# Optimization experiments

Hardware: AMD Instinct MI355X
Metric: run time of the kernel (lower is better)

## Reference

```python
import jax, jax.numpy as jnp
import numpy as np

N = 200000      # total nodes
B = 1024        # graphs
D = 256         # node_dim
OUT = 256       # out_dim


def setup_inputs() -> dict:
    key = jax.random.key(0)
    ks = jax.random.split(key, 16)
    x = jax.random.normal(ks[0], (N, D), dtype=jnp.float32)
    # sorted segment ids covering all B graphs (no empty segments)
    extra = jax.random.randint(ks[1], (N - B,), 0, B)
    batch = jnp.sort(jnp.concatenate([jnp.arange(B, dtype=jnp.int32), extra.astype(jnp.int32)]))
    # one-hot node type mask [N, 3]
    types = jax.random.randint(ks[2], (N,), 0, 3)
    node_type_mask = jax.nn.one_hot(types, 3, dtype=jnp.int32)
    s = 1.0 / np.sqrt(D)
    # attn_weight: Linear(D, D//2) -> Tanh -> Linear(D//2, 1)
    aw1 = jax.random.uniform(ks[3], (D, D // 2), jnp.float32, -s, s)
    ab1 = jnp.zeros((D // 2,), jnp.float32)
    aw2 = jax.random.uniform(ks[4], (D // 2, 1), jnp.float32, -s, s)
    ab2 = jnp.zeros((1,), jnp.float32)
    # three typed transforms Linear(D, D)
    we = jax.random.uniform(ks[5], (D, D), jnp.float32, -s, s)
    be = jnp.zeros((D,), jnp.float32)
    wv = jax.random.uniform(ks[6], (D, D), jnp.float32, -s, s)
    bv = jnp.zeros((D,), jnp.float32)
    wp = jax.random.uniform(ks[7], (D, D), jnp.float32, -s, s)
    bp = jnp.zeros((D,), jnp.float32)
    # readout MLP: Linear(3D, 2*OUT) -> SiLU -> (Dropout eval) -> Linear(2*OUT, OUT)
    w1 = jax.random.uniform(ks[8], (3 * D, 2 * OUT), jnp.float32, -1.0 / np.sqrt(3 * D), 1.0 / np.sqrt(3 * D))
    b1 = jnp.zeros((2 * OUT,), jnp.float32)
    w2 = jax.random.uniform(ks[9], (2 * OUT, OUT), jnp.float32, -1.0 / np.sqrt(2 * OUT), 1.0 / np.sqrt(2 * OUT))
    b2 = jnp.zeros((OUT,), jnp.float32)
    return dict(x=x, batch=batch, node_type_mask=node_type_mask, num_segments=B,
                aw1=aw1, ab1=ab1, aw2=aw2, ab2=ab2, we=we, be=be, wv=wv, bv=bv,
                wp=wp, bp=bp, w1=w1, b1=b1, w2=w2, b2=b2)


def reference(x, batch, node_type_mask, num_segments,
              aw1, ab1, aw2, ab2, we, be, wv, bv, wp, bp, w1, b1, w2, b2):
    nseg = int(num_segments)
    # global_mean_pool
    counts = jax.ops.segment_sum(jnp.ones((x.shape[0],), x.dtype), batch, num_segments=nseg)
    mean_pool = jax.ops.segment_sum(x, batch, num_segments=nseg) / counts[:, None]
    # attention scores + segment softmax
    scores = jnp.tanh(x @ aw1 + ab1) @ aw2 + ab2            # [N, 1]
    s = scores[:, 0]
    m = jax.ops.segment_max(s, batch, num_segments=nseg)    # [B]
    e = jnp.exp(s - m[batch])
    z = jax.ops.segment_sum(e, batch, num_segments=nseg)
    attn = e / z[batch]                                     # [N]
    attn_pool = jax.ops.segment_sum(x * attn[:, None], batch, num_segments=nseg)
    # typed physical pooling (node_type_mask path)
    mask = node_type_mask.astype(x.dtype)
    typed_x = (mask[:, 0:1] * (x @ we + be)
               + mask[:, 1:2] * (x @ wv + bv)
               + mask[:, 2:3] * (x @ wp + bp))
    phys_pool = jax.ops.segment_sum(typed_x, batch, num_segments=nseg)
    combined = jnp.concatenate([mean_pool, attn_pool, phys_pool], axis=-1)  # [B, 3D]
    h = jax.nn.silu(combined @ w1 + b1)                     # dropout = identity (eval)
    return h @ w2 + b2                                      # [B, OUT]
```

## Files before the change

### kernel.cpp

```cpp
#include <hip/hip_runtime.h>

typedef float  f32x4  __attribute__((ext_vector_type(4)));
typedef short  s16x8  __attribute__((ext_vector_type(8)));
typedef short  s16x4  __attribute__((ext_vector_type(4)));

__device__ __forceinline__ short f2bf(float f) {
  unsigned u = __float_as_uint(f);
  u += 0x7fffu + ((u >> 16) & 1u);
  return (short)(u >> 16);
}
__device__ __forceinline__ float bf2f(unsigned short us) {
  return __uint_as_float(((unsigned)us) << 16);
}
__device__ __forceinline__ float tanh_fast(float x) {
  const float e = __expf(2.0f * x);
  return 1.0f - 2.0f / (e + 1.0f);
}

__global__ __launch_bounds__(256) void k_cvtw(
    const float* __restrict__ aw1, const float* __restrict__ we, const float* __restrict__ wv,
    const float* __restrict__ wp, const float* __restrict__ w1, const float* __restrict__ w2,
    unsigned short* __restrict__ Awt, unsigned short* __restrict__ Wpt,
    unsigned short* __restrict__ W1t, unsigned short* __restrict__ W2t) {
  const int b = blockIdx.x, tid = threadIdx.x;
  if (b < 128) {
    const int e = b * 256 + tid, n = e >> 8, k = e & 255;
    Awt[e] = (unsigned short)f2bf(aw1[k * 128 + n]);
  } else if (b < 896) {
    const int e = (b - 128) * 256 + tid, n = e / 768, k = e % 768;
    const int part = k >> 8, kk = k & 255;
    const float* W = (part == 0) ? we : ((part == 1) ? wv : wp);
    Wpt[e] = (unsigned short)f2bf(W[kk * 256 + n]);
  } else if (b < 2432) {
    const int e = (b - 896) * 256 + tid, n = e / 768, k = e % 768;
    W1t[e] = (unsigned short)f2bf(w1[k * 512 + n]);
  } else {
    const int e = (b - 2432) * 256 + tid, n = e >> 9, k = e & 511;
    W2t[e] = (unsigned short)f2bf(w2[k * 256 + n]);
  }
}

__global__ __launch_bounds__(256) void k_score_pool(
    const float* __restrict__ x, const int* __restrict__ batch, const int* __restrict__ mask,
    const unsigned short* __restrict__ Awt, const float* __restrict__ ab1,
    const float* __restrict__ aw2, const float* __restrict__ ab2,
    float* __restrict__ P, float* __restrict__ EX, float* __restrict__ ZC,
    int nnodes) {
  __shared__ __align__(16) short xs[2][32][264];
  __shared__ __align__(16) float sred[4][32];
  __shared__ __align__(16) float e_sh[4][32];
  __shared__ int st_all[320];

  const int tid  = threadIdx.x;
  const int lane = tid & 63;
  const int w    = tid >> 6;
  const int quad = lane >> 4;
  const int l15  = lane & 15;

  s16x8 bfrag[8][2];
  float ab1v[2], aw2v[2];
#pragma unroll
  for (int ct = 0; ct < 2; ++ct) {
    const int col = w * 32 + ct * 16 + l15;
    ab1v[ct] = ab1[col];
    aw2v[ct] = aw2[col];
    const s16x8* bp = reinterpret_cast<const s16x8*>(Awt + (size_t)col * 256);
#pragma unroll
    for (int kt = 0; kt < 8; ++kt) bfrag[kt][ct] = bp[kt * 4 + quad];
  }
  const float ab2v = ab2[0];

  const int tiles = nnodes >> 5;
  const int tpb   = (tiles + (int)gridDim.x - 1) / (int)gridDim.x;
  const int t_beg = blockIdx.x * tpb;
  const int t_end = min(t_beg + tpb, tiles);
  if (t_beg >= t_end) return;

  {
    const int nodes0 = t_beg * 32, nblk = (t_end - t_beg) * 32;
    for (int i = tid; i < nblk; i += 256) {
      const int g = nodes0 + i;
      st_all[i] = batch[g] * 4 + mask[g * 3 + 1] + 2 * mask[g * 3 + 2];
    }
  }

  f32x4 stg[8];
  auto load_regs = [&](int tile) {
    const f32x4* xp = reinterpret_cast<const f32x4*>(x + (size_t)tile * 8192);
#pragma unroll
    for (int i = 0; i < 8; ++i) stg[i] = xp[tid + 256 * i];
  };
  const int col4 = (tid & 63) * 4;
  auto cvt_write = [&](int b) {
#pragma unroll
    for (int i = 0; i < 8; ++i) {
      const int row = (tid >> 6) + 4 * i;
      s16x4 v; v[0] = f2bf(stg[i][0]); v[1] = f2bf(stg[i][1]);
      v[2] = f2bf(stg[i][2]); v[3] = f2bf(stg[i][3]);
      *reinterpret_cast<s16x4*>(&xs[b][row][col4]) = v;
    }
  };

  load_regs(t_beg);
  cvt_write(0);
  __syncthreads();

  float a0 = 0.f, a1 = 0.f, a2 = 0.f, aex = 0.f, zc = 0.f;
  int cur = -1;

  auto flush = [&]() {
    atomicAdd(&P[cur * 768 + tid], a0);
    atomicAdd(&P[cur * 768 + 256 + tid], a1);
    atomicAdd(&P[cur * 768 + 512 + tid], a2);
    atomicAdd(&EX[cur * 256 + tid], aex);
    if (tid < 4) atomicAdd(&ZC[cur * 4 + tid], zc);
    a0 = a1 = a2 = aex = zc = 0.f;
  };

  for (int tile = t_beg; tile < t_end; ++tile) {
    const int buf = (tile - t_beg) & 1;
    const bool more = (tile + 1 < t_end);
    if (more) load_regs(tile + 1);

#pragma unroll
    for (int ng = 0; ng < 2; ++ng) {
      s16x8 af[8];
#pragma unroll
      for (int kt = 0; kt < 8; ++kt)
        af[kt] = *reinterpret_cast<const s16x8*>(&xs[buf][16 * ng + l15][kt * 32 + quad * 8]);
      float part[4] = {0.f, 0.f, 0.f, 0.f};
#pragma unroll
      for (int ct = 0; ct < 2; ++ct) {
        f32x4 acc = {0.f, 0.f, 0.f, 0.f};
#pragma unroll
        for (int kt = 0; kt < 8; ++kt)
          acc = __builtin_amdgcn_mfma_f32_16x16x32_bf16(af[kt], bfrag[kt][ct], acc, 0, 0, 0);
#pragma unroll
        for (int r = 0; r < 4; ++r)
          part[r] += tanh_fast(acc[r] + ab1v[ct]) * aw2v[ct];
      }
#pragma unroll
      for (int off = 1; off < 16; off <<= 1) {
#pragma unroll
        for (int r = 0; r < 4; ++r) part[r] += __shfl_xor(part[r], off);
      }
      if (l15 == 0) {
#pragma unroll
        for (int r = 0; r < 4; ++r) sred[w][16 * ng + quad * 4 + r] = part[r];
      }
    }
    __syncthreads();

    if (lane < 32) {
      const float s = ab2v + sred[0][lane] + sred[1][lane] + sred[2][lane] + sred[3][lane];
      e_sh[w][lane] = __expf(s);
    }

    const int base = (tile - t_beg) * 32;
#pragma unroll
    for (int n = 0; n < 32; ++n) {
      const int st  = st_all[base + n];
      const int seg = st >> 2, t = st & 3;
      if (seg != cur) { if (cur >= 0) flush(); cur = seg; }
      const float e  = e_sh[w][n];
      const float xv = bf2f((unsigned short)xs[buf][n][tid]);
      aex += e * xv;
      if (t == 0) a0 += xv; else if (t == 1) a1 += xv; else a2 += xv;
      if (tid < 4) zc += (tid == 0) ? e : ((t == tid - 1) ? 1.f : 0.f);
    }

    if (more) cvt_write(buf ^ 1);
    __syncthreads();
  }
  if (cur >= 0) flush();
}

__global__ __launch_bounds__(256) void k_finalize(
    const float* __restrict__ P, const float* __restrict__ EX,
    const float* __restrict__ ZC, float* __restrict__ comb) {
  const int b = blockIdx.x, d = threadIdx.x;
  const float p0 = P[b * 768 + d], p1 = P[b * 768 + 256 + d], p2 = P[b * 768 + 512 + d];
  const float cnt = ZC[b * 4 + 1] + ZC[b * 4 + 2] + ZC[b * 4 + 3];
  comb[(size_t)b * 768 + d]       = (p0 + p1 + p2) / cnt;
  comb[(size_t)b * 768 + 256 + d] = EX[b * 256 + d] / ZC[b * 4];
}

__global__ __launch_bounds__(256) void k_phys(
    const float* __restrict__ P, const unsigned short* __restrict__ Wpt,
    const float* __restrict__ be, const float* __restrict__ bv, const float* __restrict__ bp,
    const float* __restrict__ ZC, float* __restrict__ comb) {
  __shared__ __align__(16) short as16[16][776];
  const int tid = threadIdx.x, lane = tid & 63, w = tid >> 6;
  const int quad = lane >> 4, l15 = lane & 15;
  const int rowbase = blockIdx.x * 16;
  const int col = blockIdx.y * 64 + w * 16 + l15;

  s16x8 bfr[24];
  const s16x8* bpf = reinterpret_cast<const s16x8*>(Wpt + (size_t)col * 768);
#pragma unroll
  for (int kt = 0; kt < 24; ++kt) bfr[kt] = bpf[kt * 4 + quad];

  const f32x4* ap = reinterpret_cast<const f32x4*>(P + (size_t)rowbase * 768);
#pragma unroll
  for (int i = 0; i < 12; ++i) {
    const int ci = tid + 256 * i;
    f32x4 v = ap[ci];
    const int row = ci / 192, c4 = (ci % 192) * 4;
    s16x4 b; b[0] = f2bf(v[0]); b[1] = f2bf(v[1]); b[2] = f2bf(v[2]); b[3] = f2bf(v[3]);
    *reinterpret_cast<s16x4*>(&as16[row][c4]) = b;
  }
  __syncthreads();

  f32x4 acc = {0.f, 0.f, 0.f, 0.f};
#pragma unroll
  for (int kt = 0; kt < 24; ++kt) {
    s16x8 af = *reinterpret_cast<const s16x8*>(&as16[l15][kt * 32 + quad * 8]);
    acc = __builtin_amdgcn_mfma_f32_16x16x32_bf16(af, bfr[kt], acc, 0, 0, 0);
  }
  const float ben = be[col], bvn = bv[col], bpn = bp[col];
#pragma unroll
  for (int r = 0; r < 4; ++r) {
    const int row = rowbase + quad * 4 + r;
    const float v = acc[r] + ZC[row * 4 + 1] * ben + ZC[row * 4 + 2] * bvn + ZC[row * 4 + 3] * bpn;
    comb[(size_t)row * 768 + 512 + col] = v;
  }
}

__global__ __launch_bounds__(256) void k_mlp1(
    const float* __restrict__ A, const unsigned short* __restrict__ W1t,
    const float* __restrict__ b1, float* __restrict__ H) {
  __shared__ __align__(16) short as16[16][776];
  const int tid = threadIdx.x, lane = tid & 63, w = tid >> 6;
  const int quad = lane >> 4, l15 = lane & 15;
  const int rowbase = blockIdx.x * 16;
  const int col = blockIdx.y * 64 + w * 16 + l15;

  s16x8 bfr[24];
  const s16x8* bpf = reinterpret_cast<const s16x8*>(W1t + (size_t)col * 768);
#pragma unroll
  for (int kt = 0; kt < 24; ++kt) bfr[kt] = bpf[kt * 4 + quad];

  const f32x4* ap = reinterpret_cast<const f32x4*>(A + (size_t)rowbase * 768);
#pragma unroll
  for (int i = 0; i < 12; ++i) {
    const int ci = tid + 256 * i;
    f32x4 v = ap[ci];
    const int row = ci / 192, c4 = (ci % 192) * 4;
    s16x4 b; b[0] = f2bf(v[0]); b[1] = f2bf(v[1]); b[2] = f2bf(v[2]); b[3] = f2bf(v[3]);
    *reinterpret_cast<s16x4*>(&as16[row][c4]) = b;
  }
  __syncthreads();

  f32x4 acc = {0.f, 0.f, 0.f, 0.f};
#pragma unroll
  for (int kt = 0; kt < 24; ++kt) {
    s16x8 af = *reinterpret_cast<const s16x8*>(&as16[l15][kt * 32 + quad * 8]);
    acc = __builtin_amdgcn_mfma_f32_16x16x32_bf16(af, bfr[kt], acc, 0, 0, 0);
  }
  const float bn = b1[col];
#pragma unroll
  for (int r = 0; r < 4; ++r) {
    const int row = rowbase + quad * 4 + r;
    const float v = acc[r] + bn;
    H[(size_t)row * 512 + col] = v / (1.f + __expf(-v));
  }
}

__global__ __launch_bounds__(256) void k_mlp2(
    const float* __restrict__ A, const unsigned short* __restrict__ W2t,
    const float* __restrict__ b2, float* __restrict__ out) {
  __shared__ __align__(16) short as16[16][520];
  const int tid = threadIdx.x, lane = tid & 63, w = tid >> 6;
  const int quad = lane >> 4, l15 = lane & 15;
  const int rowbase = blockIdx.x * 16;
  const int col = blockIdx.y * 64 + w * 16 + l15;

  s16x8 bfr[16];
  const s16x8* bpf = reinterpret_cast<const s16x8*>(W2t + (size_t)col * 512);
#pragma unroll
  for (int kt = 0; kt < 16; ++kt) bfr[kt] = bpf[kt * 4 + quad];

  const f32x4* ap = reinterpret_cast<const f32x4*>(A + (size_t)rowbase * 512);
#pragma unroll
  for (int i = 0; i < 8; ++i) {
    const int ci = tid + 256 * i;
    f32x4 v = ap[ci];
    const int row = ci >> 7, c4 = (ci & 127) * 4;
    s16x4 b; b[0] = f2bf(v[0]); b[1] = f2bf(v[1]); b[2] = f2bf(v[2]); b[3] = f2bf(v[3]);
    *reinterpret_cast<s16x4*>(&as16[row][c4]) = b;
  }
  __syncthreads();

  f32x4 acc = {0.f, 0.f, 0.f, 0.f};
#pragma unroll
  for (int kt = 0; kt < 16; ++kt) {
    s16x8 af = *reinterpret_cast<const s16x8*>(&as16[l15][kt * 32 + quad * 8]);
    acc = __builtin_amdgcn_mfma_f32_16x16x32_bf16(af, bfr[kt], acc, 0, 0, 0);
  }
  const float bn = b2[col];
#pragma unroll
  for (int r = 0; r < 4; ++r) {
    const int row = rowbase + quad * 4 + r;
    out[(size_t)row * 256 + col] = acc[r] + bn;
  }
}

extern "C" void kernel_launch(void* const* d_in, const int* in_sizes, int n_in,
                              void* d_out, int out_size, void* d_ws, size_t ws_size,
                              hipStream_t stream) {
  const float* x    = (const float*)d_in[0];
  const int*   batch= (const int*)  d_in[1];
  const int*   mask = (const int*)  d_in[2];
  const float* aw1  = (const float*)d_in[4];
  const float* ab1  = (const float*)d_in[5];
  const float* aw2  = (const float*)d_in[6];
  const float* ab2  = (const float*)d_in[7];
  const float* we   = (const float*)d_in[8];
  const float* be   = (const float*)d_in[9];
  const float* wv   = (const float*)d_in[10];
  const float* bv   = (const float*)d_in[11];
  const float* wp   = (const float*)d_in[12];
  const float* bp   = (const float*)d_in[13];
  const float* w1   = (const float*)d_in[14];
  const float* b1   = (const float*)d_in[15];
  const float* w2   = (const float*)d_in[16];
  const float* b2   = (const float*)d_in[17];
  float* out = (float*)d_out;
  const int nn = in_sizes[1];

  float* ws = (float*)d_ws;
  float* P    = ws;
  float* EXs  = P    + 786432;
  float* ZCs  = EXs  + 262144;
  float* comb = ZCs  + 4096;
  float* hbuf = comb + 786432;
  unsigned short* Awt = (unsigned short*)(hbuf + 524288);
  unsigned short* Wpt = Awt + 32768;
  unsigned short* W1t = Wpt + 196608;
  unsigned short* W2t = W1t + 393216;

  hipMemsetAsync(P, 0, (size_t)(786432 + 262144 + 4096) * sizeof(float), stream);

  k_cvtw      <<<2944, 256, 0, stream>>>(aw1, we, wv, wp, w1, w2, Awt, Wpt, W1t, W2t);
  k_score_pool<<<1024, 256, 0, stream>>>(x, batch, mask, Awt, ab1, aw2, ab2, P, EXs, ZCs, nn);
  k_finalize  <<<1024, 256, 0, stream>>>(P, EXs, ZCs, comb);
  k_phys      <<<dim3(64, 4), 256, 0, stream>>>(P, Wpt, be, bv, bp, ZCs, comb);
  k_mlp1      <<<dim3(64, 8), 256, 0, stream>>>(comb, W1t, b1, hbuf);
  k_mlp2      <<<dim3(64, 4), 256, 0, stream>>>(hbuf, W2t, b2, out);
}
```

Before: 371.4 us.

## Fuse finalize, typed-phys GEMM and readout MLP into one tail kernel

Replaces the four post-pooling kernels (finalize, phys GEMM, MLP layer 1, MLP layer 2) with a single 512-thread kernel per 16-row tile. Intermediates (combined features and hidden activations) stay in LDS as bf16 instead of round-tripping through global memory. This removes three launches and the comb/hbuf traffic. In exchange, only 64 blocks run, each looping over all output columns, which lowers parallelism across the GPU.

```diff
diff --git a/kernel.cpp b/kernel.cpp
--- a/kernel.cpp
+++ b/kernel.cpp
@@ -175,133 +175,113 @@
   if (cur >= 0) flush();
 }
 
-__global__ __launch_bounds__(256) void k_finalize(
-    const float* __restrict__ P, const float* __restrict__ EX,
-    const float* __restrict__ ZC, float* __restrict__ comb) {
-  const int b = blockIdx.x, d = threadIdx.x;
-  const float p0 = P[b * 768 + d], p1 = P[b * 768 + 256 + d], p2 = P[b * 768 + 512 + d];
-  const float cnt = ZC[b * 4 + 1] + ZC[b * 4 + 2] + ZC[b * 4 + 3];
-  comb[(size_t)b * 768 + d]       = (p0 + p1 + p2) / cnt;
-  comb[(size_t)b * 768 + 256 + d] = EX[b * 256 + d] / ZC[b * 4];
-}
-
-__global__ __launch_bounds__(256) void k_phys(
-    const float* __restrict__ P, const unsigned short* __restrict__ Wpt,
+__global__ __launch_bounds__(512) void k_tail(
+    const float* __restrict__ P, const float* __restrict__ EX, const float* __restrict__ ZC,
+    const unsigned short* __restrict__ Wpt, const unsigned short* __restrict__ W1t,
+    const unsigned short* __restrict__ W2t,
     const float* __restrict__ be, const float* __restrict__ bv, const float* __restrict__ bp,
-    const float* __restrict__ ZC, float* __restrict__ comb) {
-  __shared__ __align__(16) short as16[16][776];
+    const float* __restrict__ b1, const float* __restrict__ b2,
+    float* __restrict__ out) {
+  __shared__ __align__(16) short asP[16][776];
+  __shared__ __align__(16) short asC[16][776];
+  __shared__ __align__(16) short ash[16][520];
+
   const int tid = threadIdx.x, lane = tid & 63, w = tid >> 6;
   const int quad = lane >> 4, l15 = lane & 15;
   const int rowbase = blockIdx.x * 16;
-  const int col = blockIdx.y * 64 + w * 16 + l15;
-
-  s16x8 bfr[24];
-  const s16x8* bpf = reinterpret_cast<const s16x8*>(Wpt + (size_t)col * 768);
-#pragma unroll
-  for (int kt = 0; kt < 24; ++kt) bfr[kt] = bpf[kt * 4 + quad];
 
   const f32x4* ap = reinterpret_cast<const f32x4*>(P + (size_t)rowbase * 768);
 #pragma unroll
-  for (int i = 0; i < 12; ++i) {
-    const int ci = tid + 256 * i;
+  for (int i = 0; i < 6; ++i) {
+    const int ci = tid + 512 * i;
     f32x4 v = ap[ci];
     const int row = ci / 192, c4 = (ci % 192) * 4;
     s16x4 b; b[0] = f2bf(v[0]); b[1] = f2bf(v[1]); b[2] = f2bf(v[2]); b[3] = f2bf(v[3]);
-    *reinterpret_cast<s16x4*>(&as16[row][c4]) = b;
+    *reinterpret_cast<s16x4*>(&asP[row][c4]) = b;
   }
   __syncthreads();
 
-  f32x4 acc = {0.f, 0.f, 0.f, 0.f};
-#pragma unroll
-  for (int kt = 0; kt < 24; ++kt) {
-    s16x8 af = *reinterpret_cast<const s16x8*>(&as16[l15][kt * 32 + quad * 8]);
-    acc = __builtin_amdgcn_mfma_f32_16x16x32_bf16(af, bfr[kt], acc, 0, 0, 0);
-  }
-  const float ben = be[col], bvn = bv[col], bpn = bp[col];
-#pragma unroll
-  for (int r = 0; r < 4; ++r) {
-    const int row = rowbase + quad * 4 + r;
-    const float v = acc[r] + ZC[row * 4 + 1] * ben + ZC[row * 4 + 2] * bvn + ZC[row * 4 + 3] * bpn;
-    comb[(size_t)row * 768 + 512 + col] = v;
-  }
-}
-
-__global__ __launch_bounds__(256) void k_mlp1(
-    const float* __restrict__ A, const unsigned short* __restrict__ W1t,
-    const float* __restrict__ b1, float* __restrict__ H) {
-  __shared__ __align__(16) short as16[16][776];
-  const int tid = threadIdx.x, lane = tid & 63, w = tid >> 6;
-  const int quad = lane >> 4, l15 = lane & 15;
-  const int rowbase = blockIdx.x * 16;
-  const int col = blockIdx.y * 64 + w * 16 + l15;
-
-  s16x8 bfr[24];
-  const s16x8* bpf = reinterpret_cast<const s16x8*>(W1t + (size_t)col * 768);
-#pragma unroll
-  for (int kt = 0; kt < 24; ++kt) bfr[kt] = bpf[kt * 4 + quad];
-
-  const f32x4* ap = reinterpret_cast<const f32x4*>(A + (size_t)rowbase * 768);
-#pragma unroll
-  for (int i = 0; i < 12; ++i) {
-    const int ci = tid + 256 * i;
-    f32x4 v = ap[ci];
-    const int row = ci / 192, c4 = (ci % 192) * 4;
-    s16x4 b; b[0] = f2bf(v[0]); b[1] = f2bf(v[1]); b[2] = f2bf(v[2]); b[3] = f2bf(v[3]);
-    *reinterpret_cast<s16x4*>(&as16[row][c4]) = b;
+  {
+    const int d  = tid & 255;
+    const int r0 = (tid >> 8) * 8;
+#pragma unroll
+    for (int rr = 0; rr < 8; ++rr) {
+      const int r = r0 + rr, row = rowbase + r;
+      const float z   = ZC[row * 4 + 0];
+      const float cnt = ZC[row * 4 + 1] + ZC[row * 4 + 2] + ZC[row * 4 + 3];
+      const float mp  = (P[(size_t)row * 768 + d] + P[(size_t)row * 768 + 256 + d] +
+                         P[(size_t)row * 768 + 512 + d]) / cnt;
+      const float at  = EX[(size_t)row * 256 + d] / z;
+      asC[r][d]       = f2bf(mp);
+      asC[r][256 + d] = f2bf(at);
+    }
+  }
+
+#pragma unroll 1
+  for (int cg = 0; cg < 2; ++cg) {
+    const int col = cg * 128 + w * 16 + l15;
+    s16x8 bfr[24];
+    const s16x8* bpf = reinterpret_cast<const s16x8*>(Wpt + (size_t)col * 768);
+#pragma unroll
+    for (int kt = 0; kt < 24; ++kt) bfr[kt] = bpf[kt * 4 + quad];
+    f32x4 acc = {0.f, 0.f, 0.f, 0.f};
+#pragma unroll
+    for (int kt = 0; kt < 24; ++kt) {
+      s16x8 af = *reinterpret_cast<const s16x8*>(&asP[l15][kt * 32 + quad * 8]);
+      acc = __builtin_amdgcn_mfma_f32_16x16x32_bf16(af, bfr[kt], acc, 0, 0, 0);
+    }
+    const float ben = be[col], bvn = bv[col], bpn = bp[col];
+#pragma unroll
+    for (int r = 0; r < 4; ++r) {
+      const int rl = quad * 4 + r, row = rowbase + rl;
+      const float v = acc[r] + ZC[row * 4 + 1] * ben + ZC[row * 4 + 2] * bvn + ZC[row * 4 + 3] * bpn;
+      asC[rl][512 + col] = f2bf(v);
+    }
   }
   __syncthreads();
 
-  f32x4 acc = {0.f, 0.f, 0.f, 0.f};
-#pragma unroll
-  for (int kt = 0; kt < 24; ++kt) {
-    s16x8 af = *reinterpret_cast<const s16x8*>(&as16[l15][kt * 32 + quad * 8]);
-    acc = __builtin_amdgcn_mfma_f32_16x16x32_bf16(af, bfr[kt], acc, 0, 0, 0);
-  }
-  const float bn = b1[col];
-#pragma unroll
-  for (int r = 0; r < 4; ++r) {
-    const int row = rowbase + quad * 4 + r;
-    const float v = acc[r] + bn;
-    H[(size_t)row * 512 + col] = v / (1.f + __expf(-v));
-  }
-}
-
-__global__ __launch_bounds__(256) void k_mlp2(
-    const float* __restrict__ A, const unsigned short* __restrict__ W2t,
-    const float* __restrict__ b2, float* __restrict__ out) {
-  __shared__ __align__(16) short as16[16][520];
-  const int tid = threadIdx.x, lane = tid & 63, w = tid >> 6;
-  const int quad = lane >> 4, l15 = lane & 15;
-  const int rowbase = blockIdx.x * 16;
-  const int col = blockIdx.y * 64 + w * 16 + l15;
-
-  s16x8 bfr[16];
-  const s16x8* bpf = reinterpret_cast<const s16x8*>(W2t + (size_t)col * 512);
-#pragma unroll
-  for (int kt = 0; kt < 16; ++kt) bfr[kt] = bpf[kt * 4 + quad];
-
-  const f32x4* ap = reinterpret_cast<const f32x4*>(A + (size_t)rowbase * 512);
-#pragma unroll
-  for (int i = 0; i < 8; ++i) {
-    const int ci = tid + 256 * i;
-    f32x4 v = ap[ci];
-    const int row = ci >> 7, c4 = (ci & 127) * 4;
-    s16x4 b; b[0] = f2bf(v[0]); b[1] = f2bf(v[1]); b[2] = f2bf(v[2]); b[3] = f2bf(v[3]);
-    *reinterpret_cast<s16x4*>(&as16[row][c4]) = b;
+#pragma unroll 1
+  for (int cg = 0; cg < 4; ++cg) {
+    const int col = cg * 128 + w * 16 + l15;
+    s16x8 bfr[24];
+    const s16x8* bpf = reinterpret_cast<const s16x8*>(W1t + (size_t)col * 768);
+#pragma unroll
+    for (int kt = 0; kt < 24; ++kt) bfr[kt] = bpf[kt * 4 + quad];
+    f32x4 acc = {0.f, 0.f, 0.f, 0.f};
+#pragma unroll
+    for (int kt = 0; kt < 24; ++kt) {
+      s16x8 af = *reinterpret_cast<const s16x8*>(&asC[l15][kt * 32 + quad * 8]);
+      acc = __builtin_amdgcn_mfma_f32_16x16x32_bf16(af, bfr[kt], acc, 0, 0, 0);
+    }
+    const float bn = b1[col];
+#pragma unroll
+    for (int r = 0; r < 4; ++r) {
+      const int rl = quad * 4 + r;
+      const float v = acc[r] + bn;
+      ash[rl][col] = f2bf(v / (1.f + __expf(-v)));
+    }
   }
   __syncthreads();
 
-  f32x4 acc = {0.f, 0.f, 0.f, 0.f};
-#pragma unroll
-  for (int kt = 0; kt < 16; ++kt) {
-    s16x8 af = *reinterpret_cast<const s16x8*>(&as16[l15][kt * 32 + quad * 8]);
-    acc = __builtin_amdgcn_mfma_f32_16x16x32_bf16(af, bfr[kt], acc, 0, 0, 0);
-  }
-  const float bn = b2[col];
-#pragma unroll
-  for (int r = 0; r < 4; ++r) {
-    const int row = rowbase + quad * 4 + r;
-    out[(size_t)row * 256 + col] = acc[r] + bn;
+#pragma unroll 1
+  for (int cg = 0; cg < 2; ++cg) {
+    const int col = cg * 128 + w * 16 + l15;
+    s16x8 bfr[16];
+    const s16x8* bpf = reinterpret_cast<const s16x8*>(W2t + (size_t)col * 512);
+#pragma unroll
+    for (int kt = 0; kt < 16; ++kt) bfr[kt] = bpf[kt * 4 + quad];
+    f32x4 acc = {0.f, 0.f, 0.f, 0.f};
+#pragma unroll
+    for (int kt = 0; kt < 16; ++kt) {
+      s16x8 af = *reinterpret_cast<const s16x8*>(&ash[l15][kt * 32 + quad * 8]);
+      acc = __builtin_amdgcn_mfma_f32_16x16x32_bf16(af, bfr[kt], acc, 0, 0, 0);
+    }
+    const float bn = b2[col];
+#pragma unroll
+    for (int r = 0; r < 4; ++r) {
+      const int rl = quad * 4 + r;
+      out[(size_t)(rowbase + rl) * 256 + col] = acc[r] + bn;
+    }
   }
 }
 
@@ -332,9 +312,7 @@
   float* P    = ws;
   float* EXs  = P    + 786432;
   float* ZCs  = EXs  + 262144;
-  float* comb = ZCs  + 4096;
-  float* hbuf = comb + 786432;
-  unsigned short* Awt = (unsigned short*)(hbuf + 524288);
+  unsigned short* Awt = (unsigned short*)(ZCs + 4096);
   unsigned short* Wpt = Awt + 32768;
   unsigned short* W1t = Wpt + 196608;
   unsigned short* W2t = W1t + 393216;
@@ -343,8 +321,5 @@
 
   k_cvtw      <<<2944, 256, 0, stream>>>(aw1, we, wv, wp, w1, w2, Awt, Wpt, W1t, W2t);
   k_score_pool<<<1024, 256, 0, stream>>>(x, batch, mask, Awt, ab1, aw2, ab2, P, EXs, ZCs, nn);
-  k_finalize  <<<1024, 256, 0, stream>>>(P, EXs, ZCs, comb);
-  k_phys      <<<dim3(64, 4), 256, 0, stream>>>(P, Wpt, be, bv, bp, ZCs, comb);
-  k_mlp1      <<<dim3(64, 8), 256, 0, stream>>>(comb, W1t, b1, hbuf);
-  k_mlp2      <<<dim3(64, 4), 256, 0, stream>>>(hbuf, W2t, b2, out);
-}
+  k_tail      <<<64, 512, 0, stream>>>(P, EXs, ZCs, Wpt, W1t, W2t, be, bv, bp, b1, b2, out);
+}
```

Result: slower. 395.6 us (+6.5%).

## Compute segment pooling sums with MFMA over one-hot and exp-weight matrices

Applied to the files above, without the earlier changes.

Replaces the scalar per-node accumulation loop in the score/pool kernel with bf16 MFMA. A small left matrix of exp weights (split hi/lo for precision) and one-hot type indicators multiplies a transposed bf16 copy of the x tile. Each run of nodes in the same segment is handled by masking the weight matrix with a ballot-derived range, and the z/count terms are reduced with shuffles and popcounts. It also single-buffers the MFMA A tile, adds a double-buffered transposed layout, balances the tile split across blocks, and sets launch bounds for two blocks per CU. The cost is extra LDS traffic for the transposed writes and bf16 rounding in the mean and typed sums.

```diff
diff --git a/kernel.cpp b/kernel.cpp
--- a/kernel.cpp
+++ b/kernel.cpp
@@ -40,15 +40,16 @@
   }
 }
 
-__global__ __launch_bounds__(256) void k_score_pool(
+__global__ __launch_bounds__(256, 2) void k_score_pool(
     const float* __restrict__ x, const int* __restrict__ batch, const int* __restrict__ mask,
     const unsigned short* __restrict__ Awt, const float* __restrict__ ab1,
     const float* __restrict__ aw2, const float* __restrict__ ab2,
     float* __restrict__ P, float* __restrict__ EX, float* __restrict__ ZC,
     int nnodes) {
-  __shared__ __align__(16) short xs[2][32][264];
+  __shared__ __align__(16) short xs[32][264];
+  __shared__ __align__(16) short xsB[2][8192];
   __shared__ __align__(16) float sred[4][32];
-  __shared__ __align__(16) float e_sh[4][32];
+  __shared__ __align__(16) short em[16][40];
   __shared__ int st_all[320];
 
   const int tid  = threadIdx.x;
@@ -71,9 +72,8 @@
   const float ab2v = ab2[0];
 
   const int tiles = nnodes >> 5;
-  const int tpb   = (tiles + (int)gridDim.x - 1) / (int)gridDim.x;
-  const int t_beg = blockIdx.x * tpb;
-  const int t_end = min(t_beg + tpb, tiles);
+  const int t_beg = (int)(((long long)blockIdx.x * tiles) / (long long)gridDim.x);
+  const int t_end = (int)(((long long)(blockIdx.x + 1) * tiles) / (long long)gridDim.x);
   if (t_beg >= t_end) return;
 
   {
@@ -82,22 +82,33 @@
       const int g = nodes0 + i;
       st_all[i] = batch[g] * 4 + mask[g * 3 + 1] + 2 * mask[g * 3 + 2];
     }
+    for (int i = tid; i < 640; i += 256) (&em[0][0])[i] = 0;
   }
 
   f32x4 stg[8];
   auto load_regs = [&](int tile) {
     const f32x4* xp = reinterpret_cast<const f32x4*>(x + (size_t)tile * 8192);
 #pragma unroll
-    for (int i = 0; i < 8; ++i) stg[i] = xp[tid + 256 * i];
+    for (int i = 0; i < 8; ++i) stg[i] = xp[(8 * w + i) * 64 + lane];
   };
-  const int col4 = (tid & 63) * 4;
-  auto cvt_write = [&](int b) {
+  auto cvt_write = [&](int bB) {
+    s16x4 xv[8];
 #pragma unroll
     for (int i = 0; i < 8; ++i) {
-      const int row = (tid >> 6) + 4 * i;
-      s16x4 v; v[0] = f2bf(stg[i][0]); v[1] = f2bf(stg[i][1]);
-      v[2] = f2bf(stg[i][2]); v[3] = f2bf(stg[i][3]);
-      *reinterpret_cast<s16x4*>(&xs[b][row][col4]) = v;
+      xv[i][0] = f2bf(stg[i][0]); xv[i][1] = f2bf(stg[i][1]);
+      xv[i][2] = f2bf(stg[i][2]); xv[i][3] = f2bf(stg[i][3]);
+    }
+#pragma unroll
+    for (int i = 0; i < 8; ++i)
+      *reinterpret_cast<s16x4*>(&xs[8 * w + i][lane * 4]) = xv[i];
+    const int gb = (lane >> 2) * 4 + w;
+    const int lb = (lane & 3) * 4;
+#pragma unroll
+    for (int q = 0; q < 4; ++q) {
+      s16x8 v;
+#pragma unroll
+      for (int j = 0; j < 8; ++j) v[j] = xv[j][q];
+      *reinterpret_cast<s16x8*>(&xsB[bB][(gb * 16 + lb + q) * 8]) = v;
     }
   };
 
@@ -105,16 +116,31 @@
   cvt_write(0);
   __syncthreads();
 
-  float a0 = 0.f, a1 = 0.f, a2 = 0.f, aex = 0.f, zc = 0.f;
+  const f32x4 zero4 = {0.f, 0.f, 0.f, 0.f};
+  f32x4 accB[4] = {zero4, zero4, zero4, zero4};
+  float zA = 0.f, c0A = 0.f, c1A = 0.f, c2A = 0.f;
   int cur = -1;
 
-  auto flush = [&]() {
-    atomicAdd(&P[cur * 768 + tid], a0);
-    atomicAdd(&P[cur * 768 + 256 + tid], a1);
-    atomicAdd(&P[cur * 768 + 512 + tid], a2);
-    atomicAdd(&EX[cur * 256 + tid], aex);
-    if (tid < 4) atomicAdd(&ZC[cur * 4 + tid], zc);
-    a0 = a1 = a2 = aex = zc = 0.f;
+  auto flushB = [&]() {
+#pragma unroll
+    for (int c = 0; c < 4; ++c) {
+      const int col = w * 64 + c * 16 + l15;
+      if (quad == 0) {
+        atomicAdd(&EX[cur * 256 + col], accB[c][0] + accB[c][1]);
+        atomicAdd(&P[cur * 768 + col], accB[c][2]);
+        atomicAdd(&P[cur * 768 + 256 + col], accB[c][3]);
+      } else if (quad == 1) {
+        atomicAdd(&P[cur * 768 + 512 + col], accB[c][0]);
+      }
+      accB[c] = zero4;
+    }
+    if (w == 0) {
+      if (lane < 4) {
+        const float v = (lane == 0) ? zA : ((lane == 1) ? c0A : ((lane == 2) ? c1A : c2A));
+        atomicAdd(&ZC[cur * 4 + lane], v);
+      }
+      zA = c0A = c1A = c2A = 0.f;
+    }
   };
 
   for (int tile = t_beg; tile < t_end; ++tile) {
@@ -127,7 +153,7 @@
       s16x8 af[8];
 #pragma unroll
       for (int kt = 0; kt < 8; ++kt)
-        af[kt] = *reinterpret_cast<const s16x8*>(&xs[buf][16 * ng + l15][kt * 32 + quad * 8]);
+        af[kt] = *reinterpret_cast<const s16x8*>(&xs[16 * ng + l15][kt * 32 + quad * 8]);
       float part[4] = {0.f, 0.f, 0.f, 0.f};
 #pragma unroll
       for (int ct = 0; ct < 2; ++ct) {
@@ -151,28 +177,67 @@
     }
     __syncthreads();
 
+    const int base = (tile - t_beg) * 32;
+
+    float e_f = 0.f;
+    int myt = 3;
     if (lane < 32) {
       const float s = ab2v + sred[0][lane] + sred[1][lane] + sred[2][lane] + sred[3][lane];
-      e_sh[w][lane] = __expf(s);
-    }
-
-    const int base = (tile - t_beg) * 32;
-#pragma unroll
-    for (int n = 0; n < 32; ++n) {
-      const int st  = st_all[base + n];
-      const int seg = st >> 2, t = st & 3;
-      if (seg != cur) { if (cur >= 0) flush(); cur = seg; }
-      const float e  = e_sh[w][n];
-      const float xv = bf2f((unsigned short)xs[buf][n][tid]);
-      aex += e * xv;
-      if (t == 0) a0 += xv; else if (t == 1) a1 += xv; else a2 += xv;
-      if (tid < 4) zc += (tid == 0) ? e : ((t == tid - 1) ? 1.f : 0.f);
+      e_f = __expf(s);
+      const unsigned short hi = (unsigned short)f2bf(e_f);
+      const unsigned short lo = (unsigned short)f2bf(e_f - bf2f(hi));
+      myt = st_all[base + lane] & 3;
+      em[0][lane] = (short)hi;
+      em[1][lane] = (short)lo;
+      em[2][lane] = (myt == 0) ? (short)0x3f80 : (short)0;
+      em[3][lane] = (myt == 1) ? (short)0x3f80 : (short)0;
+      em[4][lane] = (myt == 2) ? (short)0x3f80 : (short)0;
+    }
+    const int myseg = (lane < 32) ? (st_all[base + lane] >> 2) : 0x7fffffff;
+
+    s16x8 emf = *reinterpret_cast<const s16x8*>(&em[l15][quad * 8]);
+    s16x8 bfB[4];
+#pragma unroll
+    for (int c = 0; c < 4; ++c)
+      bfB[c] = *reinterpret_cast<const s16x8*>(
+          &xsB[buf][(((w * 4 + c) * 4 + quad) * 16 + l15) * 8]);
+
+    int n0 = 0;
+    while (n0 < 32) {
+      const int seg = st_all[base + n0] >> 2;
+      const unsigned long long diff = __ballot(lane < 32 && myseg != seg) >> n0;
+      const int n1 = (diff == 0) ? 32 : n0 + (int)__builtin_ctzll(diff);
+      if (seg != cur) { if (cur >= 0) flushB(); cur = seg; }
+      s16x8 af;
+      const int kb = quad * 8;
+#pragma unroll
+      for (int j = 0; j < 8; ++j) {
+        const int k = kb + j;
+        af[j] = (k >= n0 && k < n1) ? emf[j] : (short)0;
+      }
+#pragma unroll
+      for (int c = 0; c < 4; ++c)
+        accB[c] = __builtin_amdgcn_mfma_f32_16x16x32_bf16(af, bfB[c], accB[c], 0, 0, 0);
+      if (w == 0) {
+        const bool inrun = (lane >= n0 && lane < n1 && lane < 32);
+        float ee = inrun ? e_f : 0.f;
+#pragma unroll
+        for (int off = 1; off < 32; off <<= 1) ee += __shfl_xor(ee, off);
+        const unsigned long long b0 = __ballot(inrun && myt == 0);
+        const unsigned long long b1 = __ballot(inrun && myt == 1);
+        const unsigned long long b2 = __ballot(inrun && myt == 2);
+        zA  += ee;
+        c0A += (float)__popcll(b0);
+        c1A += (float)__popcll(b1);
+        c2A += (float)__popcll(b2);
+      }
+      n0 = n1;
     }
 
     if (more) cvt_write(buf ^ 1);
     __syncthreads();
   }
-  if (cur >= 0) flush();
+  if (cur >= 0) flushB();
 }
 
 __global__ __launch_bounds__(256) void k_finalize(
```

Result: faster. 348.7 us (-6.1%).
